# Kernel optimization log

Hardware: AMD Instinct MI355X
Metric: run time of the kernel (lower is better)

The kernel has to match this reference:

```python
import jax, jax.numpy as jnp
import numpy as np

B_SZ = 64
SEQ = 2048
IN_DIM = 16
D_MODEL = 128
D_INNER = 256   # expand(2) * d_model
D_STATE = 16
N_LAYERS = 5
N_PARAMS = 3
IDX_PRICE, IDX_RY, IDX_GY, IDX_NY = 0, 1, 2, 3


def setup_inputs() -> dict:
    key = jax.random.key(0)
    ks = iter(jax.random.split(key, 64))
    def nrm(shape, scale=0.02):
        return jax.random.normal(next(ks), shape, jnp.float32) * scale
    inp = {}
    # forward args
    inp["origins"] = jax.random.uniform(next(ks), (B_SZ, SEQ, IN_DIM), jnp.float32, 0.5, 1.5)
    inp["x"] = jax.random.normal(next(ks), (B_SZ, SEQ, IN_DIM), jnp.float32)
    # input embedding
    inp["emb_w"] = nrm((IN_DIM, D_MODEL)); inp["emb_b"] = jnp.zeros((D_MODEL,), jnp.float32)
    # per-layer Mamba block params, stacked on leading n_layers dim
    inp["in_w"] = nrm((N_LAYERS, D_MODEL, 2 * D_INNER)); inp["in_b"] = jnp.zeros((N_LAYERS, 2 * D_INNER), jnp.float32)
    inp["xp_w"] = nrm((N_LAYERS, D_INNER, 2 * D_STATE)); inp["xp_b"] = jnp.zeros((N_LAYERS, 2 * D_STATE), jnp.float32)
    inp["dt_w"] = nrm((N_LAYERS, D_INNER, D_INNER));     inp["dt_b"] = jnp.zeros((N_LAYERS, D_INNER), jnp.float32)
    inp["out_w"] = nrm((N_LAYERS, D_INNER, D_MODEL));    inp["out_b"] = jnp.zeros((N_LAYERS, D_MODEL), jnp.float32)
    # A_log init: log(arange(1, d_state+1)) broadcast over d_inner
    a = jnp.log(jnp.arange(1, D_STATE + 1, dtype=jnp.float32))
    inp["A_log"] = jnp.broadcast_to(a, (N_LAYERS, D_INNER, D_STATE)).copy()
    inp["Dp"] = jnp.ones((N_LAYERS, D_INNER), jnp.float32)
    # layernorms
    inp["ln_g"] = jnp.ones((N_LAYERS, D_MODEL), jnp.float32)
    inp["ln_b"] = jnp.zeros((N_LAYERS, D_MODEL), jnp.float32)
    # output head: Linear(128,64) -> ReLU -> Linear(64,3) -> Sigmoid
    inp["o1_w"] = nrm((D_MODEL, D_MODEL // 2)); inp["o1_b"] = jnp.zeros((D_MODEL // 2,), jnp.float32)
    inp["o2_w"] = nrm((D_MODEL // 2, N_PARAMS)); inp["o2_b"] = jnp.zeros((N_PARAMS,), jnp.float32)
    return inp


def _silu(x):
    return x * jax.nn.sigmoid(x)


def _layernorm(x, g, b, eps=1e-5):
    mu = jnp.mean(x, axis=-1, keepdims=True)
    var = jnp.mean(jnp.square(x - mu), axis=-1, keepdims=True)
    return (x - mu) * jax.lax.rsqrt(var + eps) * g + b


def _mamba_block(x, iw, ib, xw, xb, dw, db, ow, ob, alog, d):
    # x: [B, S, D_MODEL]
    xz = x @ iw + ib                       # [B,S,2*di]
    x_proj, z = jnp.split(xz, 2, axis=-1)  # [B,S,di] each
    u = _silu(x_proj)                      # no conv path (use_conv=False)
    A = -jnp.exp(alog)                     # [di, ds]
    x_dbl = u @ xw + xb                    # [B,S,2*ds]
    Bm, Cm = jnp.split(x_dbl, 2, axis=-1)  # [B,S,ds]
    dt = jax.nn.softplus(u @ dw + db)      # [B,S,di]

    def step(h, t):
        u_t, dt_t, B_t, C_t = t            # [B,di],[B,di],[B,ds],[B,ds]
        dA = jnp.exp(dt_t[:, :, None] * A)                 # [B,di,ds]
        h = h * dA + (dt_t * u_t)[:, :, None] * B_t[:, None, :]
        y = jnp.sum(h * C_t[:, None, :], axis=-1) + d * u_t  # [B,di]
        return h, y

    h0 = jnp.zeros((u.shape[0], u.shape[2], A.shape[-1]), u.dtype)
    xs = (jnp.swapaxes(u, 0, 1), jnp.swapaxes(dt, 0, 1),
          jnp.swapaxes(Bm, 0, 1), jnp.swapaxes(Cm, 0, 1))  # seq-major
    _, ys = jax.lax.scan(step, h0, xs)     # ys: [S,B,di]
    y = jnp.swapaxes(ys, 0, 1)             # [B,S,di]
    y = y * _silu(z)
    return y @ ow + ob                     # [B,S,D_MODEL]


def _forward(origins, x, emb_w, emb_b, in_w, in_b, xp_w, xp_b, dt_w, dt_b,
             out_w, out_b, A_log, Dp, ln_g, ln_b, o1_w, o1_b, o2_w, o2_b):
    h = x @ emb_w + emb_b
    for l in range(N_LAYERS):
        res = h
        h = _mamba_block(h, in_w[l], in_b[l], xp_w[l], xp_b[l], dt_w[l], dt_b[l],
                         out_w[l], out_b[l], A_log[l], Dp[l])
        h = _layernorm(h + res, ln_g[l], ln_b[l])
    pooled = jnp.mean(h, axis=1)                         # lengths=None path
    hid = jax.nn.relu(pooled @ o1_w + o1_b)              # dropout is eval no-op
    params = jax.nn.sigmoid(hid @ o2_w + o2_b) * 2.0     # [B, 3]
    a, b, c = params[:, 0], params[:, 1], params[:, 2]
    last_1 = origins[:, -1, :]
    last_2 = origins[:, -2, :]
    price = last_1[:, IDX_PRICE]
    ry_now, ry_before = last_1[:, IDX_RY], last_2[:, IDX_RY]
    gy_now, gy_before = last_1[:, IDX_GY], last_2[:, IDX_GY]
    ny_now, ny_before = last_1[:, IDX_NY], last_2[:, IDX_NY]
    out = price * a * ry_now / ry_before * 2.0 * (
        b * jax.nn.sigmoid(gy_now - gy_before) + c * jax.nn.sigmoid(ny_now - ny_before))
    return out  # [B]


def reference(origins, x, emb_w, emb_b, in_w, in_b, xp_w, xp_b, dt_w, dt_b,
              out_w, out_b, A_log, Dp, ln_g, ln_b, o1_w, o1_b, o2_w, o2_b):
    return _forward(origins, x, emb_w, emb_b, in_w, in_b, xp_w, xp_b, dt_w, dt_b,
                    out_w, out_b, A_log, Dp, ln_g, ln_b, o1_w, o1_b, o2_w, o2_b)
```

## Files before the change

kernel.cpp:

```cpp
#include <hip/hip_runtime.h>
#include <hip/hip_bf16.h>
#include <math.h>

#define B_SZ    64
#define SEQ     2048
#define DMODEL  128
#define DINNER  256
#define DSTATE  16
#define NLAYERS 5

typedef unsigned short u16;
typedef __attribute__((ext_vector_type(8))) short bf16x8;
typedef __attribute__((ext_vector_type(4))) float f32x4;

static __device__ __forceinline__ float bf2f(u16 u){
  union { unsigned u; float f; } a; a.u = ((unsigned)u) << 16; return a.f;
}
static __device__ __forceinline__ u16 f2bf(float f){
  union { float f; unsigned u; } a; a.f = f;
  unsigned r = a.u + 0x7fffu + ((a.u >> 16) & 1u);
  return (u16)(r >> 16);
}
static __device__ __forceinline__ float sigm(float x){ return 1.f/(1.f+__expf(-x)); }
static __device__ __forceinline__ float siluf(float x){ return x/(1.f+__expf(-x)); }

#define MFMA16(a,b,c) __builtin_amdgcn_mfma_f32_16x16x32_bf16((a),(b),(c),0,0,0)

__global__ __launch_bounds__(256) void prep_kernel(
    const float* __restrict__ in_w, const float* __restrict__ xp_w,
    const float* __restrict__ dt_w, const float* __restrict__ out_w,
    u16* __restrict__ WT1, u16* __restrict__ WT2, u16* __restrict__ WT3){
  int idx = blockIdx.x*256 + threadIdx.x;
  const int n1 = NLAYERS*512*128, n2 = NLAYERS*288*256, n3 = NLAYERS*128*256;
  if (idx < n1){
    int l = idx/(512*128), r = idx%(512*128), n = r/128, k = r%128;
    WT1[idx] = f2bf(in_w[((size_t)l*128 + k)*512 + n]);
  } else if (idx < n1+n2){
    int t = idx-n1; int l=t/(288*256), r=t%(288*256), n=r/256, k=r%256;
    float v = (n<32) ? xp_w[((size_t)l*256+k)*32 + n]
                     : dt_w[((size_t)l*256+k)*256 + (n-32)];
    WT2[t] = f2bf(v);
  } else if (idx < n1+n2+n3){
    int t = idx-n1-n2; int l=t/(128*256), r=t%(128*256), n=r/256, k=r%256;
    WT3[t] = f2bf(out_w[((size_t)l*256+k)*128 + n]);
  }
}

__global__ __launch_bounds__(256) void emb_kernel(
    const float* __restrict__ x, const float* __restrict__ ew,
    const float* __restrict__ eb, u16* __restrict__ Hb){
  int idx = blockIdx.x*256 + threadIdx.x;
  int m = idx >> 7, d = idx & 127;
  float s = eb[d];
  #pragma unroll
  for (int k=0;k<16;++k) s += x[(size_t)m*16+k]*ew[k*128+d];
  Hb[(size_t)m*128+d] = f2bf(s);
}

__global__ __launch_bounds__(256) void gemm1_kernel(
    const u16* __restrict__ Hb, const u16* __restrict__ WT,
    const float* __restrict__ bias, u16* __restrict__ U, u16* __restrict__ ZS){
  const int lane = threadIdx.x & 63, wave = threadIdx.x >> 6;
  const int half = blockIdx.x & 1;
  const int m0 = (blockIdx.x >> 1)*256 + wave*64;
  const int lr = lane & 15, kg = lane >> 4;
  bf16x8 hfrag[4][4];
  const u16* hrow = Hb + (size_t)(m0+lr)*128 + kg*8;
  #pragma unroll
  for (int g=0; g<4; ++g)
    #pragma unroll
    for (int f=0; f<4; ++f)
      hfrag[g][f] = *(const bf16x8*)(hrow + g*16*128 + f*32);
  u16* const dst = half ? ZS : U;
  const u16* wrow = WT + (size_t)(half*256+lr)*128 + kg*8;
  bf16x8 wv[4];
  #pragma unroll
  for (int f=0; f<4; ++f) wv[f] = *(const bf16x8*)(wrow + f*32);
  #pragma unroll
  for (int nn=0; nn<16; ++nn){
    bf16x8 wn[4];
    if (nn < 15){
      const u16* wr2 = wrow + (size_t)(nn+1)*16*128;
      #pragma unroll
      for (int f=0; f<4; ++f) wn[f] = *(const bf16x8*)(wr2 + f*32);
    }
    f32x4 acc[4];
    #pragma unroll
    for (int g=0; g<4; ++g){
      acc[g] = (f32x4){0.f,0.f,0.f,0.f};
      #pragma unroll
      for (int f=0; f<4; ++f) acc[g] = MFMA16(wv[f], hfrag[g][f], acc[g]);
    }
    const int ncol = nn*16 + kg*4;
    float4 bs4 = *(const float4*)(bias + half*256 + ncol);
    #pragma unroll
    for (int g=0; g<4; ++g){
      const int m = m0 + g*16 + lr;
      ushort4 uv;
      uv.x = f2bf(siluf(acc[g][0]+bs4.x));
      uv.y = f2bf(siluf(acc[g][1]+bs4.y));
      uv.z = f2bf(siluf(acc[g][2]+bs4.z));
      uv.w = f2bf(siluf(acc[g][3]+bs4.w));
      *(ushort4*)(dst + (size_t)m*256 + ncol) = uv;
    }
    #pragma unroll
    for (int f=0; f<4; ++f) wv[f] = wn[f];
  }
}

__global__ __launch_bounds__(256) void gemm2_kernel(
    const u16* __restrict__ Uin, const u16* __restrict__ WT,
    const float* __restrict__ xpb, const float* __restrict__ dtb,
    u16* __restrict__ BC, u16* __restrict__ DT){
  const int lane = threadIdx.x & 63, wave = threadIdx.x >> 6;
  const int m0 = blockIdx.x*128 + wave*32;
  const int lr = lane & 15, kg = lane >> 4;
  bf16x8 hfrag[2][8];
  const u16* arow = Uin + (size_t)(m0+lr)*256 + kg*8;
  #pragma unroll
  for (int g=0; g<2; ++g)
    #pragma unroll
    for (int f=0; f<8; ++f)
      hfrag[g][f] = *(const bf16x8*)(arow + g*16*256 + f*32);
  const u16* wrow = WT + (size_t)lr*256 + kg*8;
  bf16x8 wv[8];
  #pragma unroll
  for (int f=0; f<8; ++f) wv[f] = *(const bf16x8*)(wrow + f*32);
  #pragma unroll
  for (int nn=0; nn<18; ++nn){
    bf16x8 wn[8];
    if (nn < 17){
      const u16* wr2 = wrow + (size_t)(nn+1)*16*256;
      #pragma unroll
      for (int f=0; f<8; ++f) wn[f] = *(const bf16x8*)(wr2 + f*32);
    }
    f32x4 acc[2];
    #pragma unroll
    for (int g=0; g<2; ++g){
      acc[g] = (f32x4){0.f,0.f,0.f,0.f};
      #pragma unroll
      for (int f=0; f<8; ++f) acc[g] = MFMA16(wv[f], hfrag[g][f], acc[g]);
    }
    const int col0 = nn*16 + kg*4;
    if (col0 < 32){
      float4 bs4 = *(const float4*)(xpb + col0);
      #pragma unroll
      for (int g=0; g<2; ++g){
        const int m = m0 + g*16 + lr;
        ushort4 uv;
        uv.x = f2bf(acc[g][0]+bs4.x); uv.y = f2bf(acc[g][1]+bs4.y);
        uv.z = f2bf(acc[g][2]+bs4.z); uv.w = f2bf(acc[g][3]+bs4.w);
        *(ushort4*)(BC + (size_t)m*32 + col0) = uv;
      }
    } else {
      float4 bs4 = *(const float4*)(dtb + (col0-32));
      #pragma unroll
      for (int g=0; g<2; ++g){
        const int m = m0 + g*16 + lr;
        float v0=acc[g][0]+bs4.x, v1=acc[g][1]+bs4.y;
        float v2=acc[g][2]+bs4.z, v3=acc[g][3]+bs4.w;
        ushort4 uv;
        uv.x = f2bf(fmaxf(v0,0.f) + __logf(1.f + __expf(-fabsf(v0))));
        uv.y = f2bf(fmaxf(v1,0.f) + __logf(1.f + __expf(-fabsf(v1))));
        uv.z = f2bf(fmaxf(v2,0.f) + __logf(1.f + __expf(-fabsf(v2))));
        uv.w = f2bf(fmaxf(v3,0.f) + __logf(1.f + __expf(-fabsf(v3))));
        *(ushort4*)(DT + (size_t)m*256 + (col0-32)) = uv;
      }
    }
    #pragma unroll
    for (int f=0; f<8; ++f) wv[f] = wn[f];
  }
}

static __device__ __forceinline__ void powtree(float r, float* pw){
  float p2=r*r, p3=p2*r, p4=p2*p2;
  float p5=p4*r, p6=p4*p2, p7=p4*p3, p8=p4*p4;
  pw[0]=r;  pw[1]=p2; pw[2]=p3; pw[3]=p4;
  pw[4]=p5; pw[5]=p6; pw[6]=p7; pw[7]=p8;
  pw[8]=p8*r;  pw[9]=p8*p2;  pw[10]=p8*p3;  pw[11]=p8*p4;
  pw[12]=p8*p5; pw[13]=p8*p6; pw[14]=p8*p7; pw[15]=p8*p8;
}

__global__ __launch_bounds__(256) void scan_p1(
    const u16* __restrict__ U, const u16* __restrict__ DT,
    const u16* __restrict__ BC, const float* __restrict__ Alog,
    u16* __restrict__ SGH, float* __restrict__ SDT, int nseg, int L){
  const int seg = blockIdx.x % nseg;
  const int b   = blockIdx.x / nseg;
  const int c   = threadIdx.x;
  float a2[16]; bool geo = true;
  #pragma unroll
  for (int i=0;i<16;++i){
    float A = -__expf(Alog[c*16+i]);
    a2[i] = A * 1.44269504f;
    if (fabsf(A + (float)(i+1)) > 1e-3f) geo = false;
  }
  float h[16];
  #pragma unroll
  for (int i=0;i<16;++i) h[i]=0.f;
  float sdt = 0.f;
  const size_t mbase = (size_t)b*SEQ + (size_t)seg*L;
  if (geo){
    for (int t=0;t<L;++t){
      const size_t m = mbase + t;
      float u  = bf2f(U[m*256+c]);
      float dt = bf2f(DT[m*256+c]);
      bf16x8 b0 = *(const bf16x8*)(BC + m*32);
      bf16x8 b1 = *(const bf16x8*)(BC + m*32 + 8);
      float du = dt*u; sdt += dt;
      float r = exp2f(-1.44269504f*dt);
      float pw[16]; powtree(r, pw);
      #pragma unroll
      for (int i=0;i<8;++i)  h[i]   = h[i]  *pw[i]   + du*bf2f((u16)b0[i]);
      #pragma unroll
      for (int i=8;i<16;++i) h[i]   = h[i]  *pw[i]   + du*bf2f((u16)b1[i-8]);
    }
  } else {
    for (int t=0;t<L;++t){
      const size_t m = mbase + t;
      float u  = bf2f(U[m*256+c]);
      float dt = bf2f(DT[m*256+c]);
      bf16x8 b0 = *(const bf16x8*)(BC + m*32);
      bf16x8 b1 = *(const bf16x8*)(BC + m*32 + 8);
      float du = dt*u; sdt += dt;
      #pragma unroll
      for (int i=0;i<16;++i){
        float Bv = (i<8) ? bf2f((u16)b0[i]) : bf2f((u16)b1[i-8]);
        h[i] = h[i]*exp2f(dt*a2[i]) + du*Bv;
      }
    }
  }
  const size_t kb = ((size_t)b*nseg+seg);
  #pragma unroll
  for (int i=0;i<16;++i) SGH[(kb*16+i)*256 + c] = f2bf(h[i]);
  SDT[kb*256 + c] = sdt;
}

__global__ __launch_bounds__(256) void scan_p2(
    u16* __restrict__ SGH, const float* __restrict__ SDT,
    const float* __restrict__ Alog, int nseg){
  const int i = blockIdx.x & 15, b = blockIdx.x >> 4, c = threadIdx.x;
  const float a2 = -__expf(Alog[c*16+i]) * 1.44269504f;
  float h = 0.f;
  for (int s=0;s<nseg;++s){
    const size_t kb = ((size_t)b*nseg+s);
    float sdt = SDT[kb*256 + c];
    size_t k = (kb*16+i)*256 + c;
    float hl = bf2f(SGH[k]);
    SGH[k] = f2bf(h);
    h = h*exp2f(sdt*a2) + hl;
  }
}

__global__ __launch_bounds__(256) void scan_p3(
    u16* __restrict__ UY, const u16* __restrict__ DT, const u16* __restrict__ BC,
    const u16* __restrict__ ZS, const float* __restrict__ Alog,
    const float* __restrict__ Dp, const u16* __restrict__ SGH, int nseg, int L){
  const int seg = blockIdx.x % nseg;
  const int b   = blockIdx.x / nseg;
  const int c   = threadIdx.x;
  float a2[16]; bool geo = true;
  #pragma unroll
  for (int i=0;i<16;++i){
    float A = -__expf(Alog[c*16+i]);
    a2[i] = A * 1.44269504f;
    if (fabsf(A + (float)(i+1)) > 1e-3f) geo = false;
  }
  const float Dv = Dp[c];
  const size_t kb = ((size_t)b*nseg+seg);
  float h[16];
  #pragma unroll
  for (int i=0;i<16;++i) h[i] = bf2f(SGH[(kb*16+i)*256 + c]);
  const size_t mbase = (size_t)b*SEQ + (size_t)seg*L;
  if (geo){
    for (int t=0;t<L;++t){
      const size_t m = mbase + t;
      float u  = bf2f(UY[m*256+c]);
      float dt = bf2f(DT[m*256+c]);
      float zs = bf2f(ZS[m*256+c]);
      bf16x8 b0 = *(const bf16x8*)(BC + m*32);
      bf16x8 b1 = *(const bf16x8*)(BC + m*32 + 8);
      bf16x8 c0 = *(const bf16x8*)(BC + m*32 + 16);
      bf16x8 c1 = *(const bf16x8*)(BC + m*32 + 24);
      float du = dt*u;
      float r = exp2f(-1.44269504f*dt);
      float pw[16]; powtree(r, pw);
      float s0=0.f, s1=0.f;
      #pragma unroll
      for (int i=0;i<8;++i){
        h[i] = h[i]*pw[i] + du*bf2f((u16)b0[i]);
        s0 += h[i]*bf2f((u16)c0[i]);
      }
      #pragma unroll
      for (int i=8;i<16;++i){
        h[i] = h[i]*pw[i] + du*bf2f((u16)b1[i-8]);
        s1 += h[i]*bf2f((u16)c1[i-8]);
      }
      float y = s0 + s1 + Dv*u;
      UY[m*256+c] = f2bf(y*zs);
    }
  } else {
    for (int t=0;t<L;++t){
      const size_t m = mbase + t;
      float u  = bf2f(UY[m*256+c]);
      float dt = bf2f(DT[m*256+c]);
      float zs = bf2f(ZS[m*256+c]);
      bf16x8 b0 = *(const bf16x8*)(BC + m*32);
      bf16x8 b1 = *(const bf16x8*)(BC + m*32 + 8);
      bf16x8 c0 = *(const bf16x8*)(BC + m*32 + 16);
      bf16x8 c1 = *(const bf16x8*)(BC + m*32 + 24);
      float du = dt*u;
      float s0=0.f, s1=0.f;
      #pragma unroll
      for (int i=0;i<8;++i){
        h[i] = h[i]*exp2f(dt*a2[i]) + du*bf2f((u16)b0[i]);
        s0 += h[i]*bf2f((u16)c0[i]);
      }
      #pragma unroll
      for (int i=8;i<16;++i){
        h[i] = h[i]*exp2f(dt*a2[i]) + du*bf2f((u16)b1[i-8]);
        s1 += h[i]*bf2f((u16)c1[i-8]);
      }
      float y = s0 + s1 + Dv*u;
      UY[m*256+c] = f2bf(y*zs);
    }
  }
}

__global__ __launch_bounds__(64) void scan_kernel(
    u16* UY, const u16* __restrict__ DT, const u16* __restrict__ BC,
    const u16* __restrict__ ZS, const float* __restrict__ Alog,
    const float* __restrict__ Dp){
  const int b = blockIdx.x >> 2;
  const int c = ((blockIdx.x & 3) << 6) + threadIdx.x;
  float a2[16];
  #pragma unroll
  for (int i=0;i<16;++i) a2[i] = -__expf(Alog[c*16+i]) * 1.44269504f;
  const float Dv = Dp[c];
  float h[16];
  #pragma unroll
  for (int i=0;i<16;++i) h[i]=0.f;
  const size_t mbase = (size_t)b*SEQ;
  for (int t=0;t<SEQ;++t){
    const size_t m = mbase + t;
    float u  = bf2f(UY[m*256+c]);
    float dt = bf2f(DT[m*256+c]);
    float zs = bf2f(ZS[m*256+c]);
    bf16x8 b0 = *(const bf16x8*)(BC + m*32);
    bf16x8 b1 = *(const bf16x8*)(BC + m*32 + 8);
    bf16x8 c0 = *(const bf16x8*)(BC + m*32 + 16);
    bf16x8 c1 = *(const bf16x8*)(BC + m*32 + 24);
    float du = dt*u;
    float s0=0.f, s1=0.f;
    #pragma unroll
    for (int i=0;i<8;++i){
      h[i] = h[i]*exp2f(dt*a2[i]) + du*bf2f((u16)b0[i]);
      s0 += h[i]*bf2f((u16)c0[i]);
    }
    #pragma unroll
    for (int i=8;i<16;++i){
      h[i] = h[i]*exp2f(dt*a2[i]) + du*bf2f((u16)b1[i-8]);
      s1 += h[i]*bf2f((u16)c1[i-8]);
    }
    float y = s0+s1 + Dv*u;
    UY[m*256+c] = f2bf(y*zs);
  }
}

__global__ __launch_bounds__(256) void gemm3ln_kernel(
    const u16* __restrict__ YS, const u16* __restrict__ WT,
    const float* __restrict__ ob, const float* __restrict__ g,
    const float* __restrict__ bb, u16* __restrict__ Hb){
  const int lane = threadIdx.x & 63, wave = threadIdx.x >> 6;
  const int m0 = blockIdx.x*128 + wave*32;
  const int lr = lane & 15, kg = lane >> 4;
  bf16x8 hfrag[2][8];
  const u16* arow = YS + (size_t)(m0+lr)*256 + kg*8;
  #pragma unroll
  for (int gg=0; gg<2; ++gg)
    #pragma unroll
    for (int f=0; f<8; ++f)
      hfrag[gg][f] = *(const bf16x8*)(arow + gg*16*256 + f*32);
  const u16* wrow = WT + (size_t)lr*256 + kg*8;
  bf16x8 wv[8];
  #pragma unroll
  for (int f=0; f<8; ++f) wv[f] = *(const bf16x8*)(wrow + f*32);
  ushort4 xvp[2][8];
  float s[2] = {0.f,0.f}, q[2] = {0.f,0.f};
  #pragma unroll
  for (int n=0; n<8; ++n){
    bf16x8 wn[8];
    if (n < 7){
      const u16* wr2 = wrow + (size_t)(n+1)*16*256;
      #pragma unroll
      for (int f=0; f<8; ++f) wn[f] = *(const bf16x8*)(wr2 + f*32);
    }
    const int col0 = n*16 + kg*4;
    float4 bs4 = *(const float4*)(ob + col0);
    #pragma unroll
    for (int gg=0; gg<2; ++gg){
      f32x4 acc = {0.f,0.f,0.f,0.f};
      #pragma unroll
      for (int f=0; f<8; ++f) acc = MFMA16(wv[f], hfrag[gg][f], acc);
      const size_t m = (size_t)(m0 + gg*16 + lr);
      ushort4 rs = *(const ushort4*)(Hb + m*128 + col0);
      float x0 = acc[0] + bs4.x + bf2f(rs.x);
      float x1 = acc[1] + bs4.y + bf2f(rs.y);
      float x2 = acc[2] + bs4.z + bf2f(rs.z);
      float x3 = acc[3] + bs4.w + bf2f(rs.w);
      s[gg] += (x0+x1)+(x2+x3);
      q[gg] += (x0*x0+x1*x1)+(x2*x2+x3*x3);
      ushort4 pv; pv.x=f2bf(x0); pv.y=f2bf(x1); pv.z=f2bf(x2); pv.w=f2bf(x3);
      xvp[gg][n] = pv;
    }
    #pragma unroll
    for (int f=0; f<8; ++f) wv[f] = wn[f];
  }
  #pragma unroll
  for (int gg=0; gg<2; ++gg){
    float ss = s[gg], qq = q[gg];
    ss += __shfl_xor(ss,16); qq += __shfl_xor(qq,16);
    ss += __shfl_xor(ss,32); qq += __shfl_xor(qq,32);
    float mu  = ss * 0.0078125f;
    float var = qq * 0.0078125f - mu*mu;
    float inv = rsqrtf(var + 1e-5f);
    const size_t m = (size_t)(m0 + gg*16 + lr);
    #pragma unroll
    for (int n=0;n<8;++n){
      const int col0 = n*16 + kg*4;
      float4 g4 = *(const float4*)(g  + col0);
      float4 b4 = *(const float4*)(bb + col0);
      ushort4 pv = xvp[gg][n];
      ushort4 uv;
      uv.x = f2bf((bf2f(pv.x)-mu)*inv*g4.x + b4.x);
      uv.y = f2bf((bf2f(pv.y)-mu)*inv*g4.y + b4.y);
      uv.z = f2bf((bf2f(pv.z)-mu)*inv*g4.z + b4.z);
      uv.w = f2bf((bf2f(pv.w)-mu)*inv*g4.w + b4.w);
      *(ushort4*)(Hb + m*128 + col0) = uv;
    }
  }
}

__global__ __launch_bounds__(128) void pool1_kernel(
    const u16* __restrict__ Hb, float* __restrict__ PP){
  const int blk = blockIdx.x;
  const int tc = blk & 15, b = blk >> 4;
  const int d = threadIdx.x;
  float s = 0.f;
  const size_t base = ((size_t)b*SEQ + tc*128);
  for (int t=0;t<128;++t) s += bf2f(Hb[(base+t)*128 + d]);
  PP[((size_t)b*16 + tc)*128 + d] = s;
}
__global__ __launch_bounds__(128) void pool2_kernel(
    const float* __restrict__ PP, float* __restrict__ P){
  const int b = blockIdx.x, d = threadIdx.x;
  float s = 0.f;
  #pragma unroll
  for (int tc=0;tc<16;++tc) s += PP[((size_t)b*16+tc)*128 + d];
  P[b*128 + d] = s * (1.f/SEQ);
}

__global__ __launch_bounds__(64) void head_kernel(
    const float* __restrict__ P, const float* __restrict__ o1w,
    const float* __restrict__ o1b, const float* __restrict__ o2w,
    const float* __restrict__ o2b, const float* __restrict__ origins,
    float* __restrict__ out){
  const int b = blockIdx.x;
  const int j = threadIdx.x;
  float hv = o1b[j];
  #pragma unroll 4
  for (int d=0; d<128; ++d) hv += P[b*128+d]*o1w[d*64+j];
  hv = fmaxf(hv, 0.f);
  float p0 = hv*o2w[j*3+0], p1 = hv*o2w[j*3+1], p2 = hv*o2w[j*3+2];
  #pragma unroll
  for (int o=1;o<64;o<<=1){
    p0 += __shfl_xor(p0,o); p1 += __shfl_xor(p1,o); p2 += __shfl_xor(p2,o);
  }
  if (j == 0){
    float a = 2.f*sigm(p0 + o2b[0]);
    float bb = 2.f*sigm(p1 + o2b[1]);
    float c = 2.f*sigm(p2 + o2b[2]);
    const float* l1 = origins + ((size_t)b*SEQ + (SEQ-1))*16;
    const float* l2 = origins + ((size_t)b*SEQ + (SEQ-2))*16;
    float price=l1[0], ry_n=l1[1], ry_b=l2[1], gy_n=l1[2], gy_b=l2[2], ny_n=l1[3], ny_b=l2[3];
    out[b] = price*a*ry_n/ry_b*2.f*(bb*sigm(gy_n-gy_b) + c*sigm(ny_n-ny_b));
  }
}

extern "C" void kernel_launch(void* const* d_in, const int* in_sizes, int n_in,
                              void* d_out, int out_size, void* d_ws, size_t ws_size,
                              hipStream_t stream){
  const float* origins = (const float*)d_in[0];
  const float* x      = (const float*)d_in[1];
  const float* emb_w  = (const float*)d_in[2];
  const float* emb_b  = (const float*)d_in[3];
  const float* in_w   = (const float*)d_in[4];
  const float* in_b   = (const float*)d_in[5];
  const float* xp_w   = (const float*)d_in[6];
  const float* xp_b   = (const float*)d_in[7];
  const float* dt_w   = (const float*)d_in[8];
  const float* dt_b   = (const float*)d_in[9];
  const float* out_w  = (const float*)d_in[10];
  const float* out_b  = (const float*)d_in[11];
  const float* A_log  = (const float*)d_in[12];
  const float* Dp     = (const float*)d_in[13];
  const float* ln_g   = (const float*)d_in[14];
  const float* ln_b   = (const float*)d_in[15];
  const float* o1_w   = (const float*)d_in[16];
  const float* o1_b   = (const float*)d_in[17];
  const float* o2_w   = (const float*)d_in[18];
  const float* o2_b   = (const float*)d_in[19];
  float* outp = (float*)d_out;

  auto al = [](size_t b)->size_t{ return (b + 255) & ~(size_t)255; };
  const size_t wt1_b = al((size_t)NLAYERS*512*128*2);
  const size_t wt2_b = al((size_t)NLAYERS*288*256*2);
  const size_t wt3_b = al((size_t)NLAYERS*128*256*2);
  const size_t po_b  = al((size_t)B_SZ*128*4);
  const size_t pp_b  = al((size_t)B_SZ*16*128*4);
  const size_t fixed = wt1_b + wt2_b + wt3_b + po_b + pp_b;

  int CB = 0, NSEG = 1;
  static const int cbc[7] = {64,32,16,8,4,2,1};
  size_t hb_b=0, u_b=0, bc_b=0, sgh_b=0, sdt_b=0;
  for (int i=0;i<7 && !CB;++i){
    int cb = cbc[i];
    size_t hbb = al((size_t)cb*SEQ*128*2);
    size_t uu  = al((size_t)cb*SEQ*256*2);
    size_t bb  = al((size_t)cb*SEQ*32*2);
    size_t base = fixed + hbb + 3*uu + bb;
    if (base <= ws_size){
      CB=cb; hb_b=hbb; u_b=uu; bc_b=bb;
      static const int nsc[6] = {64,32,16,8,4,2};
      for (int k=0;k<6;++k){
        size_t sgh = al((size_t)cb*nsc[k]*DSTATE*DINNER*2);
        size_t sdt = al((size_t)cb*nsc[k]*DINNER*4);
        if (base + sgh + sdt <= ws_size){ NSEG=nsc[k]; sgh_b=sgh; sdt_b=sdt; break; }
      }
    }
  }
  if (!CB) return;

  char* ws = (char*)d_ws;
  size_t off = 0;
  auto take = [&](size_t bytes)->char*{ char* p = ws + off; off += bytes; return p; };
  u16*   WT1 = (u16*)take(wt1_b);
  u16*   WT2 = (u16*)take(wt2_b);
  u16*   WT3 = (u16*)take(wt3_b);
  float* PO  = (float*)take(po_b);
  float* PP  = (float*)take(pp_b);
  u16*   Hb  = (u16*)take(hb_b);
  u16*   U   = (u16*)take(u_b);
  u16*   ZS  = (u16*)take(u_b);
  u16*   DT  = (u16*)take(u_b);
  u16*   BC  = (u16*)take(bc_b);
  u16*   SGH = NULL; float* SDT = NULL;
  if (NSEG > 1){ SGH = (u16*)take(sgh_b); SDT = (float*)take(sdt_b); }

  prep_kernel<<<3360, 256, 0, stream>>>(in_w, xp_w, dt_w, out_w, WT1, WT2, WT3);

  const int NC = B_SZ / CB;
  const int Mc = CB * SEQ;
  const int L  = SEQ / NSEG;
  for (int ci=0; ci<NC; ++ci){
    const int b0 = ci * CB;
    const size_t R0 = (size_t)b0 * SEQ;
    emb_kernel<<<(Mc*DMODEL)/256, 256, 0, stream>>>(x + R0*16, emb_w, emb_b, Hb);
    for (int l=0;l<NLAYERS;++l){
      const float* Al = A_log + (size_t)l*DINNER*DSTATE;
      gemm1_kernel<<<(Mc/256)*2, 256, 0, stream>>>(Hb, WT1 + (size_t)l*512*128,
                                                   in_b + l*512, U, ZS);
      gemm2_kernel<<<Mc/128, 256, 0, stream>>>(U, WT2 + (size_t)l*288*256,
                                               xp_b + l*32, dt_b + l*256, BC, DT);
      if (NSEG > 1){
        scan_p1<<<CB*NSEG, 256, 0, stream>>>(U, DT, BC, Al, SGH, SDT, NSEG, L);
        scan_p2<<<CB*16, 256, 0, stream>>>(SGH, SDT, Al, NSEG);
        scan_p3<<<CB*NSEG, 256, 0, stream>>>(U, DT, BC, ZS, Al, Dp + l*DINNER,
                                             SGH, NSEG, L);
      } else {
        scan_kernel<<<CB*4, 64, 0, stream>>>(U, DT, BC, ZS, Al, Dp + l*DINNER);
      }
      gemm3ln_kernel<<<Mc/128, 256, 0, stream>>>(U, WT3 + (size_t)l*128*256,
                                                 out_b + l*128, ln_g + l*128,
                                                 ln_b + l*128, Hb);
    }
    pool1_kernel<<<CB*16, 128, 0, stream>>>(Hb, PP);
    pool2_kernel<<<CB, 128, 0, stream>>>(PP, PO + (size_t)b0*128);
  }
  head_kernel<<<B_SZ, 64, 0, stream>>>(PO, o1_w, o1_b, o2_w, o2_b, origins, outp);
}
```

Baseline: 1.932 ms.

## Fuse scan pass 3 with out-projection GEMM and LayerNorm, use channel-chunked layout

Merges the final selective-scan pass into the out-projection GEMM and LayerNorm kernel. Each block now writes its 64-step y slice to shared memory and runs the MFMA GEMM from there, so the y tensor no longer makes a round trip through global memory. Activations change from row-major to a chunked layout of 16-channel slabs, so a scan thread reads contiguous 32-byte rows per timestep. The segment count is fixed at 32 and the single-pass scan fallback is removed. GEMM loads become more strided in exchange, and the fused kernel has only CB*32 blocks with shared memory use that may limit occupancy.

```diff
diff --git a/kernel.cpp b/kernel.cpp
--- a/kernel.cpp
+++ b/kernel.cpp
@@ -8,6 +8,8 @@
 #define DINNER  256
 #define DSTATE  16
 #define NLAYERS 5
+#define NSEG    32
+#define LSEG    64
 
 typedef unsigned short u16;
 typedef __attribute__((ext_vector_type(8))) short bf16x8;
@@ -48,29 +50,30 @@
 
 __global__ __launch_bounds__(256) void emb_kernel(
     const float* __restrict__ x, const float* __restrict__ ew,
-    const float* __restrict__ eb, u16* __restrict__ Hb){
+    const float* __restrict__ eb, u16* __restrict__ Hb, size_t cs){
   int idx = blockIdx.x*256 + threadIdx.x;
   int m = idx >> 7, d = idx & 127;
   float s = eb[d];
   #pragma unroll
   for (int k=0;k<16;++k) s += x[(size_t)m*16+k]*ew[k*128+d];
-  Hb[(size_t)m*128+d] = f2bf(s);
+  Hb[(size_t)(d>>4)*cs + (size_t)m*16 + (d&15)] = f2bf(s);
 }
 
 __global__ __launch_bounds__(256) void gemm1_kernel(
     const u16* __restrict__ Hb, const u16* __restrict__ WT,
-    const float* __restrict__ bias, u16* __restrict__ U, u16* __restrict__ ZS){
+    const float* __restrict__ bias, u16* __restrict__ U, u16* __restrict__ ZS,
+    size_t cs){
   const int lane = threadIdx.x & 63, wave = threadIdx.x >> 6;
   const int half = blockIdx.x & 1;
   const int m0 = (blockIdx.x >> 1)*256 + wave*64;
   const int lr = lane & 15, kg = lane >> 4;
   bf16x8 hfrag[4][4];
-  const u16* hrow = Hb + (size_t)(m0+lr)*128 + kg*8;
   #pragma unroll
   for (int g=0; g<4; ++g)
     #pragma unroll
     for (int f=0; f<4; ++f)
-      hfrag[g][f] = *(const bf16x8*)(hrow + g*16*128 + f*32);
+      hfrag[g][f] = *(const bf16x8*)(Hb + (size_t)((kg>>1)+2*f)*cs
+                                     + (size_t)(m0+g*16+lr)*16 + (kg&1)*8);
   u16* const dst = half ? ZS : U;
   const u16* wrow = WT + (size_t)(half*256+lr)*128 + kg*8;
   bf16x8 wv[4];
@@ -91,17 +94,15 @@
       #pragma unroll
       for (int f=0; f<4; ++f) acc[g] = MFMA16(wv[f], hfrag[g][f], acc[g]);
     }
-    const int ncol = nn*16 + kg*4;
-    float4 bs4 = *(const float4*)(bias + half*256 + ncol);
+    float4 bs4 = *(const float4*)(bias + half*256 + nn*16 + kg*4);
     #pragma unroll
     for (int g=0; g<4; ++g){
-      const int m = m0 + g*16 + lr;
       ushort4 uv;
       uv.x = f2bf(siluf(acc[g][0]+bs4.x));
       uv.y = f2bf(siluf(acc[g][1]+bs4.y));
       uv.z = f2bf(siluf(acc[g][2]+bs4.z));
       uv.w = f2bf(siluf(acc[g][3]+bs4.w));
-      *(ushort4*)(dst + (size_t)m*256 + ncol) = uv;
+      *(ushort4*)(dst + (size_t)nn*cs + (size_t)(m0+g*16+lr)*16 + kg*4) = uv;
     }
     #pragma unroll
     for (int f=0; f<4; ++f) wv[f] = wn[f];
@@ -111,18 +112,19 @@
 __global__ __launch_bounds__(256) void gemm2_kernel(
     const u16* __restrict__ Uin, const u16* __restrict__ WT,
     const float* __restrict__ xpb, const float* __restrict__ dtb,
-    u16* __restrict__ BC, u16* __restrict__ DT){
+    u16* __restrict__ BC, u16* __restrict__ DT, size_t cs){
   const int lane = threadIdx.x & 63, wave = threadIdx.x >> 6;
   const int m0 = blockIdx.x*128 + wave*32;
-  const int lr = lane & 15, kg = lane >> 4;
+  const int lr = lane & 15, kg = lane >> 6 ? 0 : (lane >> 4);
+  const int kgr = lane >> 4;
   bf16x8 hfrag[2][8];
-  const u16* arow = Uin + (size_t)(m0+lr)*256 + kg*8;
   #pragma unroll
   for (int g=0; g<2; ++g)
     #pragma unroll
     for (int f=0; f<8; ++f)
-      hfrag[g][f] = *(const bf16x8*)(arow + g*16*256 + f*32);
-  const u16* wrow = WT + (size_t)lr*256 + kg*8;
+      hfrag[g][f] = *(const bf16x8*)(Uin + (size_t)((kgr>>1)+2*f)*cs
+                                     + (size_t)(m0+g*16+lr)*16 + (kgr&1)*8);
+  const u16* wrow = WT + (size_t)lr*256 + kgr*8;
   bf16x8 wv[8];
   #pragma unroll
   for (int f=0; f<8; ++f) wv[f] = *(const bf16x8*)(wrow + f*32);
@@ -141,22 +143,20 @@
       #pragma unroll
       for (int f=0; f<8; ++f) acc[g] = MFMA16(wv[f], hfrag[g][f], acc[g]);
     }
-    const int col0 = nn*16 + kg*4;
+    const int col0 = nn*16 + kgr*4;
     if (col0 < 32){
       float4 bs4 = *(const float4*)(xpb + col0);
       #pragma unroll
       for (int g=0; g<2; ++g){
-        const int m = m0 + g*16 + lr;
         ushort4 uv;
         uv.x = f2bf(acc[g][0]+bs4.x); uv.y = f2bf(acc[g][1]+bs4.y);
         uv.z = f2bf(acc[g][2]+bs4.z); uv.w = f2bf(acc[g][3]+bs4.w);
-        *(ushort4*)(BC + (size_t)m*32 + col0) = uv;
+        *(ushort4*)(BC + (size_t)nn*cs + (size_t)(m0+g*16+lr)*16 + kgr*4) = uv;
       }
     } else {
       float4 bs4 = *(const float4*)(dtb + (col0-32));
       #pragma unroll
       for (int g=0; g<2; ++g){
-        const int m = m0 + g*16 + lr;
         float v0=acc[g][0]+bs4.x, v1=acc[g][1]+bs4.y;
         float v2=acc[g][2]+bs4.z, v3=acc[g][3]+bs4.w;
         ushort4 uv;
@@ -164,7 +164,7 @@
         uv.y = f2bf(fmaxf(v1,0.f) + __logf(1.f + __expf(-fabsf(v1))));
         uv.z = f2bf(fmaxf(v2,0.f) + __logf(1.f + __expf(-fabsf(v2))));
         uv.w = f2bf(fmaxf(v3,0.f) + __logf(1.f + __expf(-fabsf(v3))));
-        *(ushort4*)(DT + (size_t)m*256 + (col0-32)) = uv;
+        *(ushort4*)(DT + (size_t)(nn-2)*cs + (size_t)(m0+g*16+lr)*16 + kgr*4) = uv;
       }
     }
     #pragma unroll
@@ -184,10 +184,11 @@
 __global__ __launch_bounds__(256) void scan_p1(
     const u16* __restrict__ U, const u16* __restrict__ DT,
     const u16* __restrict__ BC, const float* __restrict__ Alog,
-    u16* __restrict__ SGH, float* __restrict__ SDT, int nseg, int L){
-  const int seg = blockIdx.x % nseg;
-  const int b   = blockIdx.x / nseg;
+    u16* __restrict__ SGH, float* __restrict__ SDT, size_t cs){
+  const int seg = blockIdx.x % NSEG;
+  const int b   = blockIdx.x / NSEG;
   const int c   = threadIdx.x;
+  const size_t coff = (size_t)(c>>4)*cs + (c&15);
   float a2[16]; bool geo = true;
   #pragma unroll
   for (int i=0;i<16;++i){
@@ -199,14 +200,14 @@
   #pragma unroll
   for (int i=0;i<16;++i) h[i]=0.f;
   float sdt = 0.f;
-  const size_t mbase = (size_t)b*SEQ + (size_t)seg*L;
+  const size_t mbase = (size_t)b*SEQ + (size_t)seg*LSEG;
   if (geo){
-    for (int t=0;t<L;++t){
+    for (int t=0;t<LSEG;++t){
       const size_t m = mbase + t;
-      float u  = bf2f(U[m*256+c]);
-      float dt = bf2f(DT[m*256+c]);
-      bf16x8 b0 = *(const bf16x8*)(BC + m*32);
-      bf16x8 b1 = *(const bf16x8*)(BC + m*32 + 8);
+      float u  = bf2f(U [coff + m*16]);
+      float dt = bf2f(DT[coff + m*16]);
+      bf16x8 b0 = *(const bf16x8*)(BC + m*16);
+      bf16x8 b1 = *(const bf16x8*)(BC + m*16 + 8);
       float du = dt*u; sdt += dt;
       float r = exp2f(-1.44269504f*dt);
       float pw[16]; powtree(r, pw);
@@ -216,12 +217,12 @@
       for (int i=8;i<16;++i) h[i]   = h[i]  *pw[i]   + du*bf2f((u16)b1[i-8]);
     }
   } else {
-    for (int t=0;t<L;++t){
+    for (int t=0;t<LSEG;++t){
       const size_t m = mbase + t;
-      float u  = bf2f(U[m*256+c]);
-      float dt = bf2f(DT[m*256+c]);
-      bf16x8 b0 = *(const bf16x8*)(BC + m*32);
-      bf16x8 b1 = *(const bf16x8*)(BC + m*32 + 8);
+      float u  = bf2f(U [coff + m*16]);
+      float dt = bf2f(DT[coff + m*16]);
+      bf16x8 b0 = *(const bf16x8*)(BC + m*16);
+      bf16x8 b1 = *(const bf16x8*)(BC + m*16 + 8);
       float du = dt*u; sdt += dt;
       #pragma unroll
       for (int i=0;i<16;++i){
@@ -230,7 +231,7 @@
       }
     }
   }
-  const size_t kb = ((size_t)b*nseg+seg);
+  const size_t kb = ((size_t)b*NSEG+seg);
   #pragma unroll
   for (int i=0;i<16;++i) SGH[(kb*16+i)*256 + c] = f2bf(h[i]);
   SDT[kb*256 + c] = sdt;
@@ -238,12 +239,12 @@
 
 __global__ __launch_bounds__(256) void scan_p2(
     u16* __restrict__ SGH, const float* __restrict__ SDT,
-    const float* __restrict__ Alog, int nseg){
+    const float* __restrict__ Alog){
   const int i = blockIdx.x & 15, b = blockIdx.x >> 4, c = threadIdx.x;
   const float a2 = -__expf(Alog[c*16+i]) * 1.44269504f;
   float h = 0.f;
-  for (int s=0;s<nseg;++s){
-    const size_t kb = ((size_t)b*nseg+s);
+  for (int s=0;s<NSEG;++s){
+    const size_t kb = ((size_t)b*NSEG+s);
     float sdt = SDT[kb*256 + c];
     size_t k = (kb*16+i)*256 + c;
     float hl = bf2f(SGH[k]);
@@ -252,203 +253,157 @@
   }
 }
 
-__global__ __launch_bounds__(256) void scan_p3(
-    u16* __restrict__ UY, const u16* __restrict__ DT, const u16* __restrict__ BC,
-    const u16* __restrict__ ZS, const float* __restrict__ Alog,
-    const float* __restrict__ Dp, const u16* __restrict__ SGH, int nseg, int L){
-  const int seg = blockIdx.x % nseg;
-  const int b   = blockIdx.x / nseg;
-  const int c   = threadIdx.x;
-  float a2[16]; bool geo = true;
-  #pragma unroll
-  for (int i=0;i<16;++i){
-    float A = -__expf(Alog[c*16+i]);
-    a2[i] = A * 1.44269504f;
-    if (fabsf(A + (float)(i+1)) > 1e-3f) geo = false;
-  }
-  const float Dv = Dp[c];
-  const size_t kb = ((size_t)b*nseg+seg);
-  float h[16];
-  #pragma unroll
-  for (int i=0;i<16;++i) h[i] = bf2f(SGH[(kb*16+i)*256 + c]);
-  const size_t mbase = (size_t)b*SEQ + (size_t)seg*L;
-  if (geo){
-    for (int t=0;t<L;++t){
-      const size_t m = mbase + t;
-      float u  = bf2f(UY[m*256+c]);
-      float dt = bf2f(DT[m*256+c]);
-      float zs = bf2f(ZS[m*256+c]);
-      bf16x8 b0 = *(const bf16x8*)(BC + m*32);
-      bf16x8 b1 = *(const bf16x8*)(BC + m*32 + 8);
-      bf16x8 c0 = *(const bf16x8*)(BC + m*32 + 16);
-      bf16x8 c1 = *(const bf16x8*)(BC + m*32 + 24);
-      float du = dt*u;
-      float r = exp2f(-1.44269504f*dt);
-      float pw[16]; powtree(r, pw);
-      float s0=0.f, s1=0.f;
-      #pragma unroll
-      for (int i=0;i<8;++i){
-        h[i] = h[i]*pw[i] + du*bf2f((u16)b0[i]);
-        s0 += h[i]*bf2f((u16)c0[i]);
+__global__ __launch_bounds__(256) void scan3ln_kernel(
+    const u16* __restrict__ U, const u16* __restrict__ DT,
+    const u16* __restrict__ BC, const u16* __restrict__ ZS,
+    const float* __restrict__ Alog, const float* __restrict__ Dp,
+    const u16* __restrict__ SGH, const u16* __restrict__ WT,
+    const float* __restrict__ ob, const float* __restrict__ gv,
+    const float* __restrict__ bbv, u16* __restrict__ Hb, size_t cs){
+  __shared__ u16 ysl[LSEG*264];
+  const int seg = blockIdx.x % NSEG;
+  const int b   = blockIdx.x / NSEG;
+  {
+    const int c = threadIdx.x;
+    const size_t coff = (size_t)(c>>4)*cs + (c&15);
+    float a2[16]; bool geo = true;
+    #pragma unroll
+    for (int i=0;i<16;++i){
+      float A = -__expf(Alog[c*16+i]);
+      a2[i] = A * 1.44269504f;
+      if (fabsf(A + (float)(i+1)) > 1e-3f) geo = false;
+    }
+    const float Dv = Dp[c];
+    const size_t kb = ((size_t)b*NSEG+seg);
+    float h[16];
+    #pragma unroll
+    for (int i=0;i<16;++i) h[i] = bf2f(SGH[(kb*16+i)*256 + c]);
+    const size_t mbase = (size_t)b*SEQ + (size_t)seg*LSEG;
+    if (geo){
+      for (int t=0;t<LSEG;++t){
+        const size_t m = mbase + t;
+        float u  = bf2f(U [coff + m*16]);
+        float dt = bf2f(DT[coff + m*16]);
+        float zs = bf2f(ZS[coff + m*16]);
+        bf16x8 b0 = *(const bf16x8*)(BC + m*16);
+        bf16x8 b1 = *(const bf16x8*)(BC + m*16 + 8);
+        bf16x8 c0 = *(const bf16x8*)(BC + cs + m*16);
+        bf16x8 c1 = *(const bf16x8*)(BC + cs + m*16 + 8);
+        float du = dt*u;
+        float r = exp2f(-1.44269504f*dt);
+        float pw[16]; powtree(r, pw);
+        float s0=0.f, s1=0.f;
+        #pragma unroll
+        for (int i=0;i<8;++i){
+          h[i] = h[i]*pw[i] + du*bf2f((u16)b0[i]);
+          s0 += h[i]*bf2f((u16)c0[i]);
+        }
+        #pragma unroll
+        for (int i=8;i<16;++i){
+          h[i] = h[i]*pw[i] + du*bf2f((u16)b1[i-8]);
+          s1 += h[i]*bf2f((u16)c1[i-8]);
+        }
+        float y = s0 + s1 + Dv*u;
+        ysl[t*264 + c] = f2bf(y*zs);
       }
-      #pragma unroll
-      for (int i=8;i<16;++i){
-        h[i] = h[i]*pw[i] + du*bf2f((u16)b1[i-8]);
-        s1 += h[i]*bf2f((u16)c1[i-8]);
+    } else {
+      for (int t=0;t<LSEG;++t){
+        const size_t m = mbase + t;
+        float u  = bf2f(U [coff + m*16]);
+        float dt = bf2f(DT[coff + m*16]);
+        float zs = bf2f(ZS[coff + m*16]);
+        bf16x8 b0 = *(const bf16x8*)(BC + m*16);
+        bf16x8 b1 = *(const bf16x8*)(BC + m*16 + 8);
+        bf16x8 c0 = *(const bf16x8*)(BC + cs + m*16);
+        bf16x8 c1 = *(const bf16x8*)(BC + cs + m*16 + 8);
+        float du = dt*u;
+        float s0=0.f, s1=0.f;
+        #pragma unroll
+        for (int i=0;i<8;++i){
+          h[i] = h[i]*exp2f(dt*a2[i]) + du*bf2f((u16)b0[i]);
+          s0 += h[i]*bf2f((u16)c0[i]);
+        }
+        #pragma unroll
+        for (int i=8;i<16;++i){
+          h[i] = h[i]*exp2f(dt*a2[i]) + du*bf2f((u16)b1[i-8]);
+          s1 += h[i]*bf2f((u16)c1[i-8]);
+        }
+        float y = s0 + s1 + Dv*u;
+        ysl[t*264 + c] = f2bf(y*zs);
       }
-      float y = s0 + s1 + Dv*u;
-      UY[m*256+c] = f2bf(y*zs);
-    }
-  } else {
-    for (int t=0;t<L;++t){
-      const size_t m = mbase + t;
-      float u  = bf2f(UY[m*256+c]);
-      float dt = bf2f(DT[m*256+c]);
-      float zs = bf2f(ZS[m*256+c]);
-      bf16x8 b0 = *(const bf16x8*)(BC + m*32);
-      bf16x8 b1 = *(const bf16x8*)(BC + m*32 + 8);
-      bf16x8 c0 = *(const bf16x8*)(BC + m*32 + 16);
-      bf16x8 c1 = *(const bf16x8*)(BC + m*32 + 24);
-      float du = dt*u;
-      float s0=0.f, s1=0.f;
-      #pragma unroll
-      for (int i=0;i<8;++i){
-        h[i] = h[i]*exp2f(dt*a2[i]) + du*bf2f((u16)b0[i]);
-        s0 += h[i]*bf2f((u16)c0[i]);
+    }
+  }
+  __syncthreads();
+  {
+    const int lane = threadIdx.x & 63, wave = threadIdx.x >> 6;
+    const int lr = lane & 15, kg = lane >> 4;
+    const int lw = wave*16 + lr;
+    const size_t m = (size_t)b*SEQ + (size_t)seg*LSEG + lw;
+    bf16x8 hfrag[8];
+    #pragma unroll
+    for (int f=0; f<8; ++f)
+      hfrag[f] = *(const bf16x8*)(&ysl[lw*264 + kg*8 + f*32]);
+    const u16* wrow = WT + (size_t)lr*256 + kg*8;
+    bf16x8 wv[8];
+    #pragma unroll
+    for (int f=0; f<8; ++f) wv[f] = *(const bf16x8*)(wrow + f*32);
+    ushort4 xvp[8];
+    float s = 0.f, q = 0.f;
+    #pragma unroll
+    for (int n=0; n<8; ++n){
+      bf16x8 wn[8];
+      if (n < 7){
+        const u16* wr2 = wrow + (size_t)(n+1)*16*256;
+        #pragma unroll
+        for (int f=0; f<8; ++f) wn[f] = *(const bf16x8*)(wr2 + f*32);
       }
-      #pragma unroll
-      for (int i=8;i<16;++i){
-        h[i] = h[i]*exp2f(dt*a2[i]) + du*bf2f((u16)b1[i-8]);
-        s1 += h[i]*bf2f((u16)c1[i-8]);
-      }
-      float y = s0 + s1 + Dv*u;
-      UY[m*256+c] = f2bf(y*zs);
-    }
-  }
-}
-
-__global__ __launch_bounds__(64) void scan_kernel(
-    u16* UY, const u16* __restrict__ DT, const u16* __restrict__ BC,
-    const u16* __restrict__ ZS, const float* __restrict__ Alog,
-    const float* __restrict__ Dp){
-  const int b = blockIdx.x >> 2;
-  const int c = ((blockIdx.x & 3) << 6) + threadIdx.x;
-  float a2[16];
-  #pragma unroll
-  for (int i=0;i<16;++i) a2[i] = -__expf(Alog[c*16+i]) * 1.44269504f;
-  const float Dv = Dp[c];
-  float h[16];
-  #pragma unroll
-  for (int i=0;i<16;++i) h[i]=0.f;
-  const size_t mbase = (size_t)b*SEQ;
-  for (int t=0;t<SEQ;++t){
-    const size_t m = mbase + t;
-    float u  = bf2f(UY[m*256+c]);
-    float dt = bf2f(DT[m*256+c]);
-    float zs = bf2f(ZS[m*256+c]);
-    bf16x8 b0 = *(const bf16x8*)(BC + m*32);
-    bf16x8 b1 = *(const bf16x8*)(BC + m*32 + 8);
-    bf16x8 c0 = *(const bf16x8*)(BC + m*32 + 16);
-    bf16x8 c1 = *(const bf16x8*)(BC + m*32 + 24);
-    float du = dt*u;
-    float s0=0.f, s1=0.f;
-    #pragma unroll
-    for (int i=0;i<8;++i){
-      h[i] = h[i]*exp2f(dt*a2[i]) + du*bf2f((u16)b0[i]);
-      s0 += h[i]*bf2f((u16)c0[i]);
-    }
-    #pragma unroll
-    for (int i=8;i<16;++i){
-      h[i] = h[i]*exp2f(dt*a2[i]) + du*bf2f((u16)b1[i-8]);
-      s1 += h[i]*bf2f((u16)c1[i-8]);
-    }
-    float y = s0+s1 + Dv*u;
-    UY[m*256+c] = f2bf(y*zs);
-  }
-}
-
-__global__ __launch_bounds__(256) void gemm3ln_kernel(
-    const u16* __restrict__ YS, const u16* __restrict__ WT,
-    const float* __restrict__ ob, const float* __restrict__ g,
-    const float* __restrict__ bb, u16* __restrict__ Hb){
-  const int lane = threadIdx.x & 63, wave = threadIdx.x >> 6;
-  const int m0 = blockIdx.x*128 + wave*32;
-  const int lr = lane & 15, kg = lane >> 4;
-  bf16x8 hfrag[2][8];
-  const u16* arow = YS + (size_t)(m0+lr)*256 + kg*8;
-  #pragma unroll
-  for (int gg=0; gg<2; ++gg)
-    #pragma unroll
-    for (int f=0; f<8; ++f)
-      hfrag[gg][f] = *(const bf16x8*)(arow + gg*16*256 + f*32);
-  const u16* wrow = WT + (size_t)lr*256 + kg*8;
-  bf16x8 wv[8];
-  #pragma unroll
-  for (int f=0; f<8; ++f) wv[f] = *(const bf16x8*)(wrow + f*32);
-  ushort4 xvp[2][8];
-  float s[2] = {0.f,0.f}, q[2] = {0.f,0.f};
-  #pragma unroll
-  for (int n=0; n<8; ++n){
-    bf16x8 wn[8];
-    if (n < 7){
-      const u16* wr2 = wrow + (size_t)(n+1)*16*256;
-      #pragma unroll
-      for (int f=0; f<8; ++f) wn[f] = *(const bf16x8*)(wr2 + f*32);
-    }
-    const int col0 = n*16 + kg*4;
-    float4 bs4 = *(const float4*)(ob + col0);
-    #pragma unroll
-    for (int gg=0; gg<2; ++gg){
       f32x4 acc = {0.f,0.f,0.f,0.f};
       #pragma unroll
-      for (int f=0; f<8; ++f) acc = MFMA16(wv[f], hfrag[gg][f], acc);
-      const size_t m = (size_t)(m0 + gg*16 + lr);
-      ushort4 rs = *(const ushort4*)(Hb + m*128 + col0);
+      for (int f=0; f<8; ++f) acc = MFMA16(wv[f], hfrag[f], acc);
+      const int col0 = n*16 + kg*4;
+      float4 bs4 = *(const float4*)(ob + col0);
+      ushort4 rs = *(const ushort4*)(Hb + (size_t)n*cs + m*16 + kg*4);
       float x0 = acc[0] + bs4.x + bf2f(rs.x);
       float x1 = acc[1] + bs4.y + bf2f(rs.y);
       float x2 = acc[2] + bs4.z + bf2f(rs.z);
       float x3 = acc[3] + bs4.w + bf2f(rs.w);
-      s[gg] += (x0+x1)+(x2+x3);
-      q[gg] += (x0*x0+x1*x1)+(x2*x2+x3*x3);
+      s += (x0+x1)+(x2+x3);
+      q += (x0*x0+x1*x1)+(x2*x2+x3*x3);
       ushort4 pv; pv.x=f2bf(x0); pv.y=f2bf(x1); pv.z=f2bf(x2); pv.w=f2bf(x3);
-      xvp[gg][n] = pv;
-    }
-    #pragma unroll
-    for (int f=0; f<8; ++f) wv[f] = wn[f];
-  }
-  #pragma unroll
-  for (int gg=0; gg<2; ++gg){
-    float ss = s[gg], qq = q[gg];
-    ss += __shfl_xor(ss,16); qq += __shfl_xor(qq,16);
-    ss += __shfl_xor(ss,32); qq += __shfl_xor(qq,32);
-    float mu  = ss * 0.0078125f;
-    float var = qq * 0.0078125f - mu*mu;
+      xvp[n] = pv;
+      #pragma unroll
+      for (int f=0; f<8; ++f) wv[f] = wn[f];
+    }
+    s += __shfl_xor(s,16); q += __shfl_xor(q,16);
+    s += __shfl_xor(s,32); q += __shfl_xor(q,32);
+    float mu  = s * 0.0078125f;
+    float var = q * 0.0078125f - mu*mu;
     float inv = rsqrtf(var + 1e-5f);
-    const size_t m = (size_t)(m0 + gg*16 + lr);
     #pragma unroll
     for (int n=0;n<8;++n){
       const int col0 = n*16 + kg*4;
-      float4 g4 = *(const float4*)(g  + col0);
-      float4 b4 = *(const float4*)(bb + col0);
-      ushort4 pv = xvp[gg][n];
+      float4 g4 = *(const float4*)(gv  + col0);
+      float4 b4 = *(const float4*)(bbv + col0);
+      ushort4 pv = xvp[n];
       ushort4 uv;
       uv.x = f2bf((bf2f(pv.x)-mu)*inv*g4.x + b4.x);
       uv.y = f2bf((bf2f(pv.y)-mu)*inv*g4.y + b4.y);
       uv.z = f2bf((bf2f(pv.z)-mu)*inv*g4.z + b4.z);
       uv.w = f2bf((bf2f(pv.w)-mu)*inv*g4.w + b4.w);
-      *(ushort4*)(Hb + m*128 + col0) = uv;
+      *(ushort4*)(Hb + (size_t)n*cs + m*16 + kg*4) = uv;
     }
   }
 }
 
 __global__ __launch_bounds__(128) void pool1_kernel(
-    const u16* __restrict__ Hb, float* __restrict__ PP){
+    const u16* __restrict__ Hb, float* __restrict__ PP, size_t cs){
   const int blk = blockIdx.x;
   const int tc = blk & 15, b = blk >> 4;
   const int d = threadIdx.x;
+  const size_t coff = (size_t)(d>>4)*cs + (d&15);
   float s = 0.f;
   const size_t base = ((size_t)b*SEQ + tc*128);
-  for (int t=0;t<128;++t) s += bf2f(Hb[(base+t)*128 + d]);
+  for (int t=0;t<128;++t) s += bf2f(Hb[coff + (base+t)*16]);
   PP[((size_t)b*16 + tc)*128 + d] = s;
 }
 __global__ __launch_bounds__(128) void pool2_kernel(
@@ -520,23 +475,19 @@
   const size_t pp_b  = al((size_t)B_SZ*16*128*4);
   const size_t fixed = wt1_b + wt2_b + wt3_b + po_b + pp_b;
 
-  int CB = 0, NSEG = 1;
+  int CB = 0;
   static const int cbc[7] = {64,32,16,8,4,2,1};
   size_t hb_b=0, u_b=0, bc_b=0, sgh_b=0, sdt_b=0;
-  for (int i=0;i<7 && !CB;++i){
+  for (int i=0;i<7;++i){
     int cb = cbc[i];
-    size_t hbb = al((size_t)cb*SEQ*128*2);
-    size_t uu  = al((size_t)cb*SEQ*256*2);
-    size_t bb  = al((size_t)cb*SEQ*32*2);
-    size_t base = fixed + hbb + 3*uu + bb;
-    if (base <= ws_size){
-      CB=cb; hb_b=hbb; u_b=uu; bc_b=bb;
-      static const int nsc[6] = {64,32,16,8,4,2};
-      for (int k=0;k<6;++k){
-        size_t sgh = al((size_t)cb*nsc[k]*DSTATE*DINNER*2);
-        size_t sdt = al((size_t)cb*nsc[k]*DINNER*4);
-        if (base + sgh + sdt <= ws_size){ NSEG=nsc[k]; sgh_b=sgh; sdt_b=sdt; break; }
-      }
+    size_t csz = (size_t)cb*SEQ*16;
+    size_t hbb = al(8*csz*2);
+    size_t uu  = al(16*csz*2);
+    size_t bb  = al(2*csz*2);
+    size_t sgh = al((size_t)cb*NSEG*DSTATE*DINNER*2);
+    size_t sdt = al((size_t)cb*NSEG*DINNER*4);
+    if (fixed + hbb + 3*uu + bb + sgh + sdt <= ws_size){
+      CB=cb; hb_b=hbb; u_b=uu; bc_b=bb; sgh_b=sgh; sdt_b=sdt; break;
     }
   }
   if (!CB) return;
@@ -554,37 +505,32 @@
   u16*   ZS  = (u16*)take(u_b);
   u16*   DT  = (u16*)take(u_b);
   u16*   BC  = (u16*)take(bc_b);
-  u16*   SGH = NULL; float* SDT = NULL;
-  if (NSEG > 1){ SGH = (u16*)take(sgh_b); SDT = (float*)take(sdt_b); }
+  u16*   SGH = (u16*)take(sgh_b);
+  float* SDT = (float*)take(sdt_b);
 
   prep_kernel<<<3360, 256, 0, stream>>>(in_w, xp_w, dt_w, out_w, WT1, WT2, WT3);
 
   const int NC = B_SZ / CB;
   const int Mc = CB * SEQ;
-  const int L  = SEQ / NSEG;
+  const size_t cs = (size_t)Mc*16;
   for (int ci=0; ci<NC; ++ci){
     const int b0 = ci * CB;
     const size_t R0 = (size_t)b0 * SEQ;
-    emb_kernel<<<(Mc*DMODEL)/256, 256, 0, stream>>>(x + R0*16, emb_w, emb_b, Hb);
+    emb_kernel<<<(Mc*DMODEL)/256, 256, 0, stream>>>(x + R0*16, emb_w, emb_b, Hb, cs);
     for (int l=0;l<NLAYERS;++l){
       const float* Al = A_log + (size_t)l*DINNER*DSTATE;
       gemm1_kernel<<<(Mc/256)*2, 256, 0, stream>>>(Hb, WT1 + (size_t)l*512*128,
-                                                   in_b + l*512, U, ZS);
+                                                   in_b + l*512, U, ZS, cs);
       gemm2_kernel<<<Mc/128, 256, 0, stream>>>(U, WT2 + (size_t)l*288*256,
-                                               xp_b + l*32, dt_b + l*256, BC, DT);
-      if (NSEG > 1){
-        scan_p1<<<CB*NSEG, 256, 0, stream>>>(U, DT, BC, Al, SGH, SDT, NSEG, L);
-        scan_p2<<<CB*16, 256, 0, stream>>>(SGH, SDT, Al, NSEG);
-        scan_p3<<<CB*NSEG, 256, 0, stream>>>(U, DT, BC, ZS, Al, Dp + l*DINNER,
-                                             SGH, NSEG, L);
-      } else {
-        scan_kernel<<<CB*4, 64, 0, stream>>>(U, DT, BC, ZS, Al, Dp + l*DINNER);
-      }
-      gemm3ln_kernel<<<Mc/128, 256, 0, stream>>>(U, WT3 + (size_t)l*128*256,
-                                                 out_b + l*128, ln_g + l*128,
-                                                 ln_b + l*128, Hb);
-    }
-    pool1_kernel<<<CB*16, 128, 0, stream>>>(Hb, PP);
+                                               xp_b + l*32, dt_b + l*256, BC, DT, cs);
+      scan_p1<<<CB*NSEG, 256, 0, stream>>>(U, DT, BC, Al, SGH, SDT, cs);
+      scan_p2<<<CB*16, 256, 0, stream>>>(SGH, SDT, Al);
+      scan3ln_kernel<<<CB*NSEG, 256, 0, stream>>>(U, DT, BC, ZS, Al, Dp + l*DINNER,
+                                                  SGH, WT3 + (size_t)l*128*256,
+                                                  out_b + l*128, ln_g + l*128,
+                                                  ln_b + l*128, Hb, cs);
+    }
+    pool1_kernel<<<CB*16, 128, 0, stream>>>(Hb, PP, cs);
     pool2_kernel<<<CB, 128, 0, stream>>>(PP, PO + (size_t)b0*128);
   }
   head_kernel<<<B_SZ, 64, 0, stream>>>(PO, o1_w, o1_b, o2_w, o2_b, origins, outp);
```

After: 1.955 ms. About the same (+1.2%).
